# Kernel tuning notes

Measured on AMD Instinct MI355X. Metric: run time of the kernel, lower is better.

## Reference

```python
import jax, jax.numpy as jnp
import numpy as np

C = 256
C8 = C // 8


def setup_inputs() -> dict:
    key = jax.random.key(0)
    ks = jax.random.split(key, 9)
    B, H, W = 4, 64, 64
    s = 1.0 / np.sqrt(C)
    return {
        "pre_feat": jax.random.normal(ks[0], (B, C, H, W), jnp.float32),
        "post_feat": jax.random.normal(ks[1], (B, C, H, W), jnp.float32),
        "Wq": jax.random.normal(ks[2], (C8, C), jnp.float32) * s,
        "bq": jnp.zeros((C8,), jnp.float32),
        "Wk": jax.random.normal(ks[3], (C8, C), jnp.float32) * s,
        "bk": jnp.zeros((C8,), jnp.float32),
        "Wv": jax.random.normal(ks[4], (C, C), jnp.float32) * s,
        "bv": jnp.zeros((C,), jnp.float32),
        "gamma": jnp.zeros((1,), jnp.float32),
    }


def reference(pre_feat, post_feat, Wq, bq, Wk, bk, Wv, bv, gamma):
    B, Cc, H, W = pre_feat.shape
    N = H * W
    pre = pre_feat.reshape(B, Cc, N)    # (B, C, N)
    post = post_feat.reshape(B, Cc, N)
    # 1x1 convs == per-pixel linear projections
    q = jnp.einsum('dc,bcn->bdn', Wq, post) + bq[None, :, None]  # (B, C8, N)
    k = jnp.einsum('dc,bcn->bdn', Wk, pre) + bk[None, :, None]   # (B, C8, N)
    v = jnp.einsum('dc,bcn->bdn', Wv, pre) + bv[None, :, None]   # (B, C, N)
    # energy[b,i,j] = <q[b,:,i], k[b,:,j]>  (unscaled)
    energy = jnp.einsum('bdi,bdj->bij', q, k)                    # (B, N, N)
    attention = jax.nn.softmax(energy, axis=-1)
    # out[b,c,i] = sum_j v[b,c,j] * attention[b,i,j]
    out = jnp.einsum('bcj,bij->bci', v, attention).reshape(B, Cc, H, W)
    return gamma[0] * out + post_feat
```

## Files before the change

kernel.cpp:

```cpp
#include <hip/hip_runtime.h>
#include <hip/hip_bf16.h>

#define Bn 4
#define Cn 256
#define Dn 32
#define Nn 4096

typedef __bf16 bf16x8 __attribute__((ext_vector_type(8)));
typedef float f32x4 __attribute__((ext_vector_type(4)));

__device__ __forceinline__ float bf2f(unsigned short u) {
  unsigned int v = ((unsigned int)u) << 16;
  return __builtin_bit_cast(float, v);
}
__device__ __forceinline__ unsigned short f2bf(float f) {
  unsigned int v = __builtin_bit_cast(unsigned int, f);
  v += 0x7FFFu + ((v >> 16) & 1u);
  return (unsigned short)(v >> 16);
}
__device__ __forceinline__ unsigned int pk2(float a, float b) {
  union { __hip_bfloat162 h; unsigned int u; } x;
  x.h = __float22bfloat162_rn(make_float2(a, b));
  return x.u;
}
__device__ __forceinline__ bf16x8 ldfrag(const unsigned short* p) {
  return __builtin_bit_cast(bf16x8, *(const uint4*)p);
}
__device__ __forceinline__ uint4 pack8(const float* p) {
  float4 a = *(const float4*)p;
  float4 b = *(const float4*)(p + 4);
  union { unsigned int u2[4]; uint4 u; } x;
  x.u2[0] = pk2(a.x, a.y); x.u2[1] = pk2(a.z, a.w);
  x.u2[2] = pk2(b.x, b.y); x.u2[3] = pk2(b.z, b.w);
  return x.u;
}
__device__ __forceinline__ void async16(unsigned short* lds, const unsigned short* g) {
  __builtin_amdgcn_global_load_lds(
      (const __attribute__((address_space(1))) unsigned int*)g,
      (__attribute__((address_space(3))) unsigned int*)lds, 16, 0, 0);
}

__global__ __launch_bounds__(256) void wconv(
    const float* __restrict__ Wq, const float* __restrict__ Wk,
    const float* __restrict__ Wv,
    unsigned short* __restrict__ WqBf, unsigned short* __restrict__ WkBf,
    unsigned short* __restrict__ WvBf)
{
  const size_t base = ((size_t)blockIdx.x * 256 + threadIdx.x) * 8;
  if (base < 8192) {
    *(uint4*)(WqBf + base) = pack8(Wq + base);
  } else if (base < 16384) {
    *(uint4*)(WkBf + base - 8192) = pack8(Wk + base - 8192);
  } else {
    *(uint4*)(WvBf + base - 16384) = pack8(Wv + base - 16384);
  }
}

__global__ __launch_bounds__(256) void qkprep(
    const float* __restrict__ pre, const float* __restrict__ post,
    const unsigned short* __restrict__ WqBf, const float* __restrict__ bq,
    const unsigned short* __restrict__ WkBf, const float* __restrict__ bk,
    const unsigned short* __restrict__ WvBf, const float* __restrict__ bv,
    unsigned short* __restrict__ Qt, unsigned short* __restrict__ Kt,
    unsigned short* __restrict__ VBf)
{
  __shared__ __align__(16) unsigned short sV[256 * 24];

  const int tid = threadIdx.x;
  const int lane = tid & 63, w = tid >> 6;
  const int quad = lane >> 4, n16 = lane & 15;
  const int b = blockIdx.x >> 8;
  const int i0 = (blockIdx.x & 255) << 4;
  const int i = i0 + n16;
  const int cbase = w * 64;

  const f32x4 zz = {0.f, 0.f, 0.f, 0.f};
  f32x4 accv[4];
#pragma unroll
  for (int ct = 0; ct < 4; ct++) accv[ct] = zz;
  f32x4 aqk0 = zz, aqk1 = zz;

  const float* postB = post + (size_t)b * Cn * Nn + i;
  const float* preB  = pre  + (size_t)b * Cn * Nn + i;

#pragma unroll
  for (int kc = 0; kc < 8; kc++) {
    const int c0 = kc * 32 + quad * 8;
    const float* pr = preB + (size_t)c0 * Nn;
    union { unsigned int u2[4]; bf16x8 v; } bq8;
#pragma unroll
    for (int e2 = 0; e2 < 4; e2++) {
      float r0 = pr[(size_t)(2 * e2) * Nn], r1 = pr[(size_t)(2 * e2 + 1) * Nn];
      bq8.u2[e2] = pk2(r0, r1);
    }
    if (w == 0) {
      const float* pp = postB + (size_t)c0 * Nn;
      union { unsigned int u2[4]; bf16x8 v; } bp;
#pragma unroll
      for (int e2 = 0; e2 < 4; e2++) {
        float p0 = pp[(size_t)(2 * e2) * Nn], p1 = pp[(size_t)(2 * e2 + 1) * Nn];
        bp.u2[e2] = pk2(p0, p1);
      }
      bf16x8 awq0 = ldfrag(WqBf + (size_t)(n16) * Cn + kc * 32 + quad * 8);
      bf16x8 awq1 = ldfrag(WqBf + (size_t)(16 + n16) * Cn + kc * 32 + quad * 8);
      aqk0 = __builtin_amdgcn_mfma_f32_16x16x32_bf16(awq0, bp.v, aqk0, 0, 0, 0);
      aqk1 = __builtin_amdgcn_mfma_f32_16x16x32_bf16(awq1, bp.v, aqk1, 0, 0, 0);
    } else if (w == 1) {
      bf16x8 awk0 = ldfrag(WkBf + (size_t)(n16) * Cn + kc * 32 + quad * 8);
      bf16x8 awk1 = ldfrag(WkBf + (size_t)(16 + n16) * Cn + kc * 32 + quad * 8);
      aqk0 = __builtin_amdgcn_mfma_f32_16x16x32_bf16(awk0, bq8.v, aqk0, 0, 0, 0);
      aqk1 = __builtin_amdgcn_mfma_f32_16x16x32_bf16(awk1, bq8.v, aqk1, 0, 0, 0);
    }
#pragma unroll
    for (int ct = 0; ct < 4; ct++) {
      bf16x8 aw = ldfrag(WvBf + (size_t)(cbase + ct * 16 + n16) * Cn + kc * 32 + quad * 8);
      accv[ct] = __builtin_amdgcn_mfma_f32_16x16x32_bf16(aw, bq8.v, accv[ct], 0, 0, 0);
    }
  }

  const float LOG2E = 1.44269504f;
  if (w == 0) {
#pragma unroll
    for (int dh = 0; dh < 2; dh++) {
      const f32x4 a = dh ? aqk1 : aqk0;
      union { unsigned short s[4]; uint2 u; } oq;
#pragma unroll
      for (int r = 0; r < 4; r++)
        oq.s[r] = f2bf((a[r] + bq[dh * 16 + quad * 4 + r]) * LOG2E);
      *(uint2*)(Qt + ((size_t)b * Nn + i) * Dn + dh * 16 + quad * 4) = oq.u;
    }
  } else if (w == 1) {
#pragma unroll
    for (int dh = 0; dh < 2; dh++) {
      const f32x4 a = dh ? aqk1 : aqk0;
      union { unsigned short s[4]; uint2 u; } ok;
#pragma unroll
      for (int r = 0; r < 4; r++)
        ok.s[r] = f2bf(a[r] + bk[dh * 16 + quad * 4 + r]);
      *(uint2*)(Kt + ((size_t)b * Nn + i) * Dn + dh * 16 + quad * 4) = ok.u;
    }
  }

#pragma unroll
  for (int ct = 0; ct < 4; ct++) {
#pragma unroll
    for (int r = 0; r < 4; r++) {
      const int c = cbase + ct * 16 + quad * 4 + r;
      sV[c * 24 + n16] = f2bf(accv[ct][r] + bv[c]);
    }
  }
  __syncthreads();
#pragma unroll
  for (int pass = 0; pass < 2; pass++) {
    const int slot = tid + pass * 256;
    const int c = slot >> 1, half = slot & 1;
    *(uint4*)(VBf + ((size_t)b * Cn + c) * Nn + i0 + half * 8) =
        *(const uint4*)(sV + c * 24 + half * 8);
  }
}

__global__ __launch_bounds__(256, 4) void flash_attn(
    const unsigned short* __restrict__ Qt, const unsigned short* __restrict__ Kt,
    const unsigned short* __restrict__ VBf,
    unsigned short* __restrict__ Opart, float* __restrict__ Lpart)
{
  __shared__ __align__(16) unsigned short sX[256 * 64];
  __shared__ __align__(16) unsigned short Pl[64 * 64];

  const int tid = threadIdx.x;
  const int lane = tid & 63, w = tid >> 6;
  const int quad = lane >> 4, n16 = lane & 15;
  const int bid = blockIdx.x;
  const int pair = bid & 7, sub = bid >> 3;
  const int b  = pair >> 1;
  const int js = ((pair & 1) << 1) | (sub >> 6);
  const int it = sub & 63;
  const int i0 = it * 64;
  const int jbase = js * 1024;

  const bf16x8 qf = ldfrag(Qt + ((size_t)b * Nn + i0 + w * 16 + n16) * Dn + quad * 8);

  const f32x4 zz = {0.f, 0.f, 0.f, 0.f};
  f32x4 acc[4][4];
#pragma unroll
  for (int sub2 = 0; sub2 < 4; sub2++)
#pragma unroll
    for (int ct = 0; ct < 4; ct++) acc[sub2][ct] = zz;
  float lrow = 0.f;

  const size_t laneoff = (size_t)(lane >> 3) * Nn + (size_t)(((lane & 7) ^ (lane >> 3)) << 3);
  const unsigned short* preB = VBf + (size_t)b * Cn * Nn + laneoff;
  const int xsw = n16 & 7;
  const int xoff0 = (quad ^ xsw) << 3;
  const int xoff1 = ((4 + quad) ^ xsw) << 3;
  const int psw = (n16 & 7) << 3;

  for (int t = 0; t < 16; ++t) {
    const int j0 = jbase + t * 64;
    __syncthreads();
#pragma unroll
    for (int k = 0; k < 8; k++) {
      const int rb = (k * 4 + w) * 8;
      async16(sX + rb * 64 + (lane << 3), preB + (size_t)rb * Nn + j0);
    }
    {
      f32x4 sc[4];
#pragma unroll
      for (int jt = 0; jt < 4; jt++) {
        bf16x8 akf = ldfrag(Kt + ((size_t)b * Nn + j0 + jt * 16 + n16) * Dn + quad * 8);
        sc[jt] = __builtin_amdgcn_mfma_f32_16x16x32_bf16(akf, qf, zz, 0, 0, 0);
      }
      float ps = 0.f;
#pragma unroll
      for (int jt = 0; jt < 4; jt++) {
        float p0 = exp2f(fminf(sc[jt][0], 101.f));
        float p1 = exp2f(fminf(sc[jt][1], 101.f));
        float p2 = exp2f(fminf(sc[jt][2], 101.f));
        float p3 = exp2f(fminf(sc[jt][3], 101.f));
        ps += (p0 + p1) + (p2 + p3);
        union { unsigned int u2[2]; uint2 u; } pk;
        pk.u2[0] = pk2(p0, p1);
        pk.u2[1] = pk2(p2, p3);
        *(uint2*)&Pl[(size_t)(w * 16 + n16) * 64 + ((jt * 16 + quad * 4) ^ psw)] = pk.u;
      }
      ps += __shfl_xor(ps, 16);
      ps += __shfl_xor(ps, 32);
      lrow += ps;
    }
    __syncthreads();

    __builtin_amdgcn_s_setprio(1);
#pragma unroll
    for (int kc = 0; kc < 2; kc++) {
      const int xo = kc ? xoff1 : xoff0;
      bf16x8 pB[4];
#pragma unroll
      for (int sub2 = 0; sub2 < 4; sub2++)
        pB[sub2] = ldfrag(&Pl[(size_t)(sub2 * 16 + n16) * 64 + ((kc * 32 + quad * 8) ^ psw)]);
#pragma unroll
      for (int ct = 0; ct < 4; ct++) {
        const int crow = w * 64 + ct * 16 + n16;
        bf16x8 av = ldfrag(&sX[crow * 64 + xo]);
        acc[0][ct] = __builtin_amdgcn_mfma_f32_16x16x32_bf16(av, pB[0], acc[0][ct], 0, 0, 0);
        acc[1][ct] = __builtin_amdgcn_mfma_f32_16x16x32_bf16(av, pB[1], acc[1][ct], 0, 0, 0);
        acc[2][ct] = __builtin_amdgcn_mfma_f32_16x16x32_bf16(av, pB[2], acc[2][ct], 0, 0, 0);
        acc[3][ct] = __builtin_amdgcn_mfma_f32_16x16x32_bf16(av, pB[3], acc[3][ct], 0, 0, 0);
      }
    }
    __builtin_amdgcn_s_setprio(0);
  }

  const size_t pbase = (size_t)(js * 4 + b) * Nn;
  if (quad == 0) Lpart[pbase + i0 + w * 16 + n16] = lrow;
#pragma unroll
  for (int sub2 = 0; sub2 < 4; sub2++) {
    const int i = i0 + sub2 * 16 + n16;
#pragma unroll
    for (int ct = 0; ct < 4; ct++) {
      union { unsigned int u2[2]; uint2 u; } pk;
      pk.u2[0] = pk2(acc[sub2][ct][0], acc[sub2][ct][1]);
      pk.u2[1] = pk2(acc[sub2][ct][2], acc[sub2][ct][3]);
      *(uint2*)(Opart + (pbase + i) * 256 + w * 64 + ct * 16 + quad * 4) = pk.u;
    }
  }
}

__global__ __launch_bounds__(256) void combine(
    const unsigned short* __restrict__ Opart, const float* __restrict__ Lpart,
    const float* __restrict__ post, const float* __restrict__ gamma,
    float* __restrict__ out)
{
  __shared__ float sT[64 * 65];
  __shared__ float sL[64];

  const int tid = threadIdx.x;
  const int b = blockIdx.x >> 8;
  const int rest = blockIdx.x & 255;
  const int i0 = (rest >> 2) * 64;
  const int c0 = (rest & 3) * 64;

  if (tid < 64) {
    float l = 0.f;
#pragma unroll
    for (int js = 0; js < 4; js++) l += Lpart[(size_t)(js * 4 + b) * Nn + i0 + tid];
    sL[tid] = 1.f / l;
  }
  __syncthreads();

#pragma unroll
  for (int pass = 0; pass < 2; pass++) {
    const int il = (tid >> 3) + pass * 32;
    const int c8 = (tid & 7) << 3;
    float a[8] = {0.f, 0.f, 0.f, 0.f, 0.f, 0.f, 0.f, 0.f};
#pragma unroll
    for (int js = 0; js < 4; js++) {
      uint4 uu = *(const uint4*)(Opart + ((size_t)(js * 4 + b) * Nn + i0 + il) * 256 + c0 + c8);
      const unsigned short* us = (const unsigned short*)&uu;
#pragma unroll
      for (int e = 0; e < 8; e++) a[e] += bf2f(us[e]);
    }
    const float inv = sL[il];
#pragma unroll
    for (int e = 0; e < 8; e++) sT[(c8 + e) * 65 + il] = a[e] * inv;
  }
  __syncthreads();

  const float g = gamma[0];
#pragma unroll
  for (int itr = 0; itr < 4; itr++) {
    const int slot = tid + itr * 256;
    const int cr = slot >> 4, i4 = (slot & 15) << 2;
    const size_t addr = ((size_t)b * Cn + c0 + cr) * Nn + i0 + i4;
    float4 pp = *(const float4*)(post + addr);
    float4 ov;
    ov.x = g * sT[cr * 65 + i4 + 0] + pp.x;
    ov.y = g * sT[cr * 65 + i4 + 1] + pp.y;
    ov.z = g * sT[cr * 65 + i4 + 2] + pp.z;
    ov.w = g * sT[cr * 65 + i4 + 3] + pp.w;
    *(float4*)(out + addr) = ov;
  }
}

extern "C" void kernel_launch(void* const* d_in, const int* in_sizes, int n_in,
                              void* d_out, int out_size, void* d_ws, size_t ws_size,
                              hipStream_t stream) {
  const float* pre   = (const float*)d_in[0];
  const float* post  = (const float*)d_in[1];
  const float* Wq    = (const float*)d_in[2];
  const float* bq    = (const float*)d_in[3];
  const float* Wk    = (const float*)d_in[4];
  const float* bk    = (const float*)d_in[5];
  const float* Wv    = (const float*)d_in[6];
  const float* bv    = (const float*)d_in[7];
  const float* gamma = (const float*)d_in[8];
  float* out = (float*)d_out;

  unsigned short* ws = (unsigned short*)d_ws;
  unsigned short* Qt    = ws;
  unsigned short* Kt    = Qt + (size_t)Bn * Nn * Dn;
  unsigned short* VBf   = Kt + (size_t)Bn * Nn * Dn;
  unsigned short* WqBf  = VBf + (size_t)Bn * Cn * Nn;
  unsigned short* WkBf  = WqBf + Dn * Cn;
  unsigned short* WvBf  = WkBf + Dn * Cn;
  float* Lpart = (float*)(WvBf + Cn * Cn);
  unsigned short* Opart = (unsigned short*)(Lpart + 4 * Bn * Nn);

  wconv<<<40, 256, 0, stream>>>(Wq, Wk, Wv, WqBf, WkBf, WvBf);
  qkprep<<<1024, 256, 0, stream>>>(pre, post, WqBf, bq, WkBf, bk, WvBf, bv,
                                   Qt, Kt, VBf);
  flash_attn<<<1024, 256, 0, stream>>>(Qt, Kt, VBf, Opart, Lpart);
  combine<<<1024, 256, 0, stream>>>(Opart, Lpart, post, gamma, out);
}
```

Baseline: 190.5 us.

## Rebalance qkprep work split across pixels, channel halves and warps

Each qkprep block now covers 32 pixels and half of the V output channels, with every warp doing one Q or K MFMA chain plus four V tiles. Before, warps 0 and 1 carried the extra Q/K projection work and the other two warps sat idle for it. The grid size stays the same, but pre-activations are now read twice (once per channel half), and post is read only by half==0 blocks. The aim is to remove the per-warp load imbalance in the projection kernel and widen the VBf stores to 64-byte rows.

```diff
diff --git a/kernel.cpp b/kernel.cpp
--- a/kernel.cpp
+++ b/kernel.cpp
@@ -64,98 +64,92 @@
     unsigned short* __restrict__ Qt, unsigned short* __restrict__ Kt,
     unsigned short* __restrict__ VBf)
 {
-  __shared__ __align__(16) unsigned short sV[256 * 24];
+  __shared__ __align__(16) unsigned short sV[128 * 40];
 
   const int tid = threadIdx.x;
   const int lane = tid & 63, w = tid >> 6;
   const int quad = lane >> 4, n16 = lane & 15;
+  const int half = blockIdx.x & 1;
+  const int it = (blockIdx.x >> 1) & 127;
   const int b = blockIdx.x >> 8;
-  const int i0 = (blockIdx.x & 255) << 4;
-  const int i = i0 + n16;
-  const int cbase = w * 64;
+  const int i0 = it << 5;
+  const int isub = w & 1, ch = w >> 1;
+  const int i = i0 + isub * 16 + n16;
 
   const f32x4 zz = {0.f, 0.f, 0.f, 0.f};
+  f32x4 aqk = zz;
   f32x4 accv[4];
 #pragma unroll
   for (int ct = 0; ct < 4; ct++) accv[ct] = zz;
-  f32x4 aqk0 = zz, aqk1 = zz;
 
   const float* postB = post + (size_t)b * Cn * Nn + i;
   const float* preB  = pre  + (size_t)b * Cn * Nn + i;
 
 #pragma unroll
   for (int kc = 0; kc < 8; kc++) {
-    const int c0 = kc * 32 + quad * 8;
-    const float* pr = preB + (size_t)c0 * Nn;
+    const int co = kc * 32 + quad * 8;
+    const float* pr = preB + (size_t)co * Nn;
     union { unsigned int u2[4]; bf16x8 v; } bq8;
 #pragma unroll
     for (int e2 = 0; e2 < 4; e2++) {
       float r0 = pr[(size_t)(2 * e2) * Nn], r1 = pr[(size_t)(2 * e2 + 1) * Nn];
       bq8.u2[e2] = pk2(r0, r1);
     }
-    if (w == 0) {
-      const float* pp = postB + (size_t)c0 * Nn;
+    if (half == 0) {
+      const float* pp = postB + (size_t)co * Nn;
       union { unsigned int u2[4]; bf16x8 v; } bp;
 #pragma unroll
       for (int e2 = 0; e2 < 4; e2++) {
         float p0 = pp[(size_t)(2 * e2) * Nn], p1 = pp[(size_t)(2 * e2 + 1) * Nn];
         bp.u2[e2] = pk2(p0, p1);
       }
-      bf16x8 awq0 = ldfrag(WqBf + (size_t)(n16) * Cn + kc * 32 + quad * 8);
-      bf16x8 awq1 = ldfrag(WqBf + (size_t)(16 + n16) * Cn + kc * 32 + quad * 8);
-      aqk0 = __builtin_amdgcn_mfma_f32_16x16x32_bf16(awq0, bp.v, aqk0, 0, 0, 0);
-      aqk1 = __builtin_amdgcn_mfma_f32_16x16x32_bf16(awq1, bp.v, aqk1, 0, 0, 0);
-    } else if (w == 1) {
-      bf16x8 awk0 = ldfrag(WkBf + (size_t)(n16) * Cn + kc * 32 + quad * 8);
-      bf16x8 awk1 = ldfrag(WkBf + (size_t)(16 + n16) * Cn + kc * 32 + quad * 8);
-      aqk0 = __builtin_amdgcn_mfma_f32_16x16x32_bf16(awk0, bq8.v, aqk0, 0, 0, 0);
-      aqk1 = __builtin_amdgcn_mfma_f32_16x16x32_bf16(awk1, bq8.v, aqk1, 0, 0, 0);
+      bf16x8 awq = ldfrag(WqBf + (size_t)(ch * 16 + n16) * Cn + co);
+      aqk = __builtin_amdgcn_mfma_f32_16x16x32_bf16(awq, bp.v, aqk, 0, 0, 0);
+    } else {
+      bf16x8 awk = ldfrag(WkBf + (size_t)(ch * 16 + n16) * Cn + co);
+      aqk = __builtin_amdgcn_mfma_f32_16x16x32_bf16(awk, bq8.v, aqk, 0, 0, 0);
     }
 #pragma unroll
     for (int ct = 0; ct < 4; ct++) {
-      bf16x8 aw = ldfrag(WvBf + (size_t)(cbase + ct * 16 + n16) * Cn + kc * 32 + quad * 8);
+      bf16x8 aw = ldfrag(WvBf + (size_t)(half * 128 + ch * 64 + ct * 16 + n16) * Cn + co);
       accv[ct] = __builtin_amdgcn_mfma_f32_16x16x32_bf16(aw, bq8.v, accv[ct], 0, 0, 0);
     }
   }
 
   const float LOG2E = 1.44269504f;
-  if (w == 0) {
-#pragma unroll
-    for (int dh = 0; dh < 2; dh++) {
-      const f32x4 a = dh ? aqk1 : aqk0;
-      union { unsigned short s[4]; uint2 u; } oq;
-#pragma unroll
-      for (int r = 0; r < 4; r++)
-        oq.s[r] = f2bf((a[r] + bq[dh * 16 + quad * 4 + r]) * LOG2E);
-      *(uint2*)(Qt + ((size_t)b * Nn + i) * Dn + dh * 16 + quad * 4) = oq.u;
-    }
-  } else if (w == 1) {
-#pragma unroll
-    for (int dh = 0; dh < 2; dh++) {
-      const f32x4 a = dh ? aqk1 : aqk0;
-      union { unsigned short s[4]; uint2 u; } ok;
-#pragma unroll
-      for (int r = 0; r < 4; r++)
-        ok.s[r] = f2bf(a[r] + bk[dh * 16 + quad * 4 + r]);
-      *(uint2*)(Kt + ((size_t)b * Nn + i) * Dn + dh * 16 + quad * 4) = ok.u;
-    }
+  if (half == 0) {
+    union { unsigned short s[4]; uint2 u; } oq;
+#pragma unroll
+    for (int r = 0; r < 4; r++) {
+      const int d = ch * 16 + quad * 4 + r;
+      oq.s[r] = f2bf((aqk[r] + bq[d]) * LOG2E);
+    }
+    *(uint2*)(Qt + ((size_t)b * Nn + i) * Dn + ch * 16 + quad * 4) = oq.u;
+  } else {
+    union { unsigned short s[4]; uint2 u; } ok;
+#pragma unroll
+    for (int r = 0; r < 4; r++) {
+      const int d = ch * 16 + quad * 4 + r;
+      ok.s[r] = f2bf(aqk[r] + bk[d]);
+    }
+    *(uint2*)(Kt + ((size_t)b * Nn + i) * Dn + ch * 16 + quad * 4) = ok.u;
   }
 
 #pragma unroll
   for (int ct = 0; ct < 4; ct++) {
 #pragma unroll
     for (int r = 0; r < 4; r++) {
-      const int c = cbase + ct * 16 + quad * 4 + r;
-      sV[c * 24 + n16] = f2bf(accv[ct][r] + bv[c]);
+      const int cl = ch * 64 + ct * 16 + quad * 4 + r;
+      sV[cl * 40 + isub * 16 + n16] = f2bf(accv[ct][r] + bv[half * 128 + cl]);
     }
   }
   __syncthreads();
 #pragma unroll
   for (int pass = 0; pass < 2; pass++) {
     const int slot = tid + pass * 256;
-    const int c = slot >> 1, half = slot & 1;
-    *(uint4*)(VBf + ((size_t)b * Cn + c) * Nn + i0 + half * 8) =
-        *(const uint4*)(sV + c * 24 + half * 8);
+    const int c = slot >> 2, seg = slot & 3;
+    *(uint4*)(VBf + ((size_t)b * Cn + half * 128 + c) * Nn + i0 + seg * 8) =
+        *(const uint4*)(sV + c * 40 + seg * 8);
   }
 }
 
```

Measured after the change: 183.2 us. 3.8% less time.
